# Kernel optimization log

Measured on AMD Instinct MI355X. Metric: run time of the kernel, lower is better.

## Reference

```python
import jax, jax.numpy as jnp
import numpy as np

N = 50000   # nodes
E = 600000  # edges (avg degree 12)
D = 128     # embedding_dim == hidden_features
L = 4       # depth


def setup_inputs() -> dict:
    key = jax.random.key(0)
    k0, k1, k2, k3 = jax.random.split(key, 4)
    scale = 1.0 / np.sqrt(D)
    node_embedding = jax.random.normal(k0, (N, D), jnp.float32)
    edge_index = jax.random.randint(k1, (2, E), 0, N, dtype=jnp.int32)
    Ws_rel = jax.random.normal(k2, (L, D, D), jnp.float32) * scale
    bs_rel = jnp.zeros((L, D), jnp.float32)
    Ws_root = jax.random.normal(k3, (L, D, D), jnp.float32) * scale
    return {
        'node_embedding': node_embedding,
        'edge_index': edge_index,
        'Ws_rel': Ws_rel,
        'bs_rel': bs_rel,
        'Ws_root': Ws_root,
    }


def reference(node_embedding, edge_index, Ws_rel, bs_rel, Ws_root):
    # PyG GraphConv (aggr='mean'), flow source_to_target:
    #   out_i = lin_rel(mean_{j in N(i)} x_j) + lin_root(x_i)
    # followed by ELU (dropout probs are 0 -> identity).
    n = node_embedding.shape[0]
    src, dst = edge_index[0], edge_index[1]
    ones = jnp.ones((edge_index.shape[1],), node_embedding.dtype)
    deg = jax.ops.segment_sum(ones, dst, num_segments=n)
    inv_deg = (1.0 / jnp.maximum(deg, 1.0))[:, None]  # [n, 1]
    X = node_embedding
    for l in range(Ws_rel.shape[0]):
        agg = jax.ops.segment_sum(X[src], dst, num_segments=n) * inv_deg  # [n, D]
        out = agg @ Ws_rel[l] + bs_rel[l] + X @ Ws_root[l]
        X = jax.nn.elu(out)
    return X
```

## Files before the change

kernel.cpp:

```cpp
#include <hip/hip_runtime.h>

#define D 128
#define LDR 264
#define TR 32
#define SLOTS 64
#define EPB 2048

typedef short bf16x8 __attribute__((ext_vector_type(8)));
typedef float f32x4 __attribute__((ext_vector_type(4)));

__device__ __forceinline__ unsigned short f2bf(float f) {
  unsigned int u = __float_as_uint(f);
  unsigned int r = (u + 0x7fff + ((u >> 16) & 1)) >> 16;
  return (unsigned short)r;
}
__device__ __forceinline__ unsigned int pack2bf(float lo, float hi) {
  return (unsigned int)f2bf(lo) | ((unsigned int)f2bf(hi) << 16);
}

__global__ __launch_bounds__(256) void k_build(
    const int* __restrict__ src, const int* __restrict__ dst, int E, int N,
    int* __restrict__ cursor, unsigned short* __restrict__ csr64,
    const float* __restrict__ X0, unsigned short* __restrict__ Xb, int total4,
    const float* __restrict__ Wrel, const float* __restrict__ Wroot,
    unsigned short* __restrict__ Wp, int wtot,
    int fb, int cb) {
  int b = blockIdx.x;
  if (b < fb) {
    int p = b & 7;
    int chunk = b >> 3;
    int lo = (int)((long long)p * N / 8);
    int hi = (int)((long long)(p + 1) * N / 8);
    int base = chunk * EPB + threadIdx.x;
#pragma unroll
    for (int it = 0; it < EPB / 256; ++it, base += 256) {
      if (base < E) {
        int d = dst[base];
        if (d >= lo && d < hi) {
          int ps = atomicAdd(&cursor[d], 1);
          if (ps < SLOTS) csr64[d * SLOTS + ps] = (unsigned short)src[base];
        }
      }
    }
    return;
  }
  b -= fb;
  if (b < cb) {
    int i = b * 256 + threadIdx.x;
    if (i < total4) {
      float4 v = ((const float4*)X0)[i];
      ushort4 o;
      o.x = f2bf(v.x); o.y = f2bf(v.y); o.z = f2bf(v.z); o.w = f2bf(v.w);
      ((ushort4*)Xb)[i] = o;
    }
    return;
  }
  b -= cb;
  {
    int gid = b * 256 + threadIdx.x;
    if (gid >= wtot) return;
    int lane = gid & 63;
    int t = gid >> 6;
    int ctg = t & 7; t >>= 3;
    int ks = t & 7; t >>= 3;
    int l = t;
    const float* Wr = Wrel + (size_t)l * D * D;
    const float* Wo = Wroot + (size_t)l * D * D;
    int colc = ctg * 16 + (lane & 15);
    int krow0 = ks * 32 + (lane >> 4) * 8;
    unsigned short tmp[8];
#pragma unroll
    for (int j = 0; j < 8; ++j) {
      int kr = krow0 + j;
      float w = (kr < D) ? Wr[(size_t)kr * D + colc] : Wo[(size_t)(kr - D) * D + colc];
      tmp[j] = f2bf(w);
    }
    unsigned short* dstp = Wp + ((size_t)gid) * 8;
#pragma unroll
    for (int j = 0; j < 8; ++j) dstp[j] = tmp[j];
  }
}


#define ACC8(v) \
    acc[0] += __uint_as_float((v).x << 16); acc[1] += __uint_as_float((v).x & 0xffff0000u); \
    acc[2] += __uint_as_float((v).y << 16); acc[3] += __uint_as_float((v).y & 0xffff0000u); \
    acc[4] += __uint_as_float((v).z << 16); acc[5] += __uint_as_float((v).z & 0xffff0000u); \
    acc[6] += __uint_as_float((v).w << 16); acc[7] += __uint_as_float((v).w & 0xffff0000u);

__global__ __launch_bounds__(256, 6) void k_layer_fused(
    const unsigned short* __restrict__ Xin,
    const int* __restrict__ cursor, const unsigned short* __restrict__ csr64,
    const unsigned short* __restrict__ Wp_l, const float* __restrict__ bias,
    unsigned short* __restrict__ Xnext, float* __restrict__ out_f32,
    int last, int N) {
  __shared__ __align__(16) unsigned short sRow[TR * LDR];
  int tid = threadIdx.x;
  int r0 = blockIdx.x * TR;
  int wave = tid >> 6, lane = tid & 63;
  int grp = lane >> 4;
  int l16 = lane & 15;

  int deg[2];
  uint2 bkt[2];
  uint4 vroot[2];
#pragma unroll
  for (int s = 0; s < 2; ++s) {
    int node = r0 + wave * 8 + s * 4 + grp;
    bool val = node < N;
    deg[s] = val ? cursor[node] : 0;
    bkt[s] = val ? *(const uint2*)(csr64 + (size_t)node * SLOTS + l16 * 4)
                 : make_uint2(0u, 0u);
    vroot[s] = val ? *(const uint4*)(Xin + (size_t)node * D + l16 * 8)
                   : make_uint4(0u, 0u, 0u, 0u);
  }

#pragma unroll
  for (int s = 0; s < 2; ++s) {
    int curnode = r0 + wave * 8 + s * 4 + grp;
    int safe = (curnode < N) ? curnode : 0;
    int r = wave * 8 + s * 4 + grp;
    *(uint4*)(&sRow[r * LDR + (16 + l16) * 8]) = vroot[s];

    float acc[8];
#pragma unroll
    for (int t = 0; t < 8; ++t) acc[t] = 0.f;

    int n = min(deg[s], SLOTS);
    int j = 0;
    for (; j < n; j += 8) {
      int rem = n - j;
      int a = grp * 16 + (j >> 2);
      unsigned ua_x = (unsigned)__shfl((int)bkt[s].x, a);
      unsigned ua_y = (unsigned)__shfl((int)bkt[s].y, a);
      if (rem > 4) {
        unsigned ub_x = (unsigned)__shfl((int)bkt[s].x, a + 1);
        unsigned ub_y = (unsigned)__shfl((int)bkt[s].y, a + 1);
        int e[8];
        e[0] = (int)(ua_x & 0xffffu); e[1] = (int)(ua_x >> 16);
        e[2] = (int)(ua_y & 0xffffu); e[3] = (int)(ua_y >> 16);
        e[4] = (int)(ub_x & 0xffffu); e[5] = (int)(ub_x >> 16);
        e[6] = (int)(ub_y & 0xffffu); e[7] = (int)(ub_y >> 16);
        uint4 vv[8];
#pragma unroll
        for (int t = 0; t < 8; ++t) {
          int idx = (j + t < n) ? e[t] : safe;
          vv[t] = *(const uint4*)(Xin + (size_t)idx * D + l16 * 8);
        }
#pragma unroll
        for (int t = 0; t < 8; ++t) {
          if (j + t < n) { ACC8(vv[t]) }
        }
      } else {
        int e[4];
        e[0] = (int)(ua_x & 0xffffu); e[1] = (int)(ua_x >> 16);
        e[2] = (int)(ua_y & 0xffffu); e[3] = (int)(ua_y >> 16);
        uint4 vv[4];
#pragma unroll
        for (int t = 0; t < 4; ++t) {
          int idx = (j + t < n) ? e[t] : safe;
          vv[t] = *(const uint4*)(Xin + (size_t)idx * D + l16 * 8);
        }
#pragma unroll
        for (int t = 0; t < 4; ++t) {
          if (j + t < n) { ACC8(vv[t]) }
        }
      }
    }

    float inv = 1.0f / fmaxf((float)deg[s], 1.0f);
    uint4 o;
    o.x = pack2bf(acc[0] * inv, acc[1] * inv);
    o.y = pack2bf(acc[2] * inv, acc[3] * inv);
    o.z = pack2bf(acc[4] * inv, acc[5] * inv);
    o.w = pack2bf(acc[6] * inv, acc[7] * inv);
    *(uint4*)(&sRow[r * LDR + l16 * 8]) = o;
  }
  __syncthreads();

  int m = l16, q = grp;
  int ct0 = wave * 2;

  f32x4 cacc[2][2];
#pragma unroll
  for (int g = 0; g < 2; ++g)
#pragma unroll
    for (int c = 0; c < 2; ++c) cacc[g][c] = (f32x4){0.f, 0.f, 0.f, 0.f};

  const unsigned short* arow = &sRow[m * LDR + q * 8];
#pragma unroll
  for (int ks = 0; ks < 8; ++ks) {
    bf16x8 b0 = *(const bf16x8*)(Wp_l + ((size_t)((ks * 8 + ct0 + 0) * 64 + lane)) * 8);
    bf16x8 b1 = *(const bf16x8*)(Wp_l + ((size_t)((ks * 8 + ct0 + 1) * 64 + lane)) * 8);
    bf16x8 a0 = *(const bf16x8*)(arow + ks * 32);
    bf16x8 a1 = *(const bf16x8*)(arow + 16 * LDR + ks * 32);
    cacc[0][0] = __builtin_amdgcn_mfma_f32_16x16x32_bf16(a0, b0, cacc[0][0], 0, 0, 0);
    cacc[0][1] = __builtin_amdgcn_mfma_f32_16x16x32_bf16(a0, b1, cacc[0][1], 0, 0, 0);
    cacc[1][0] = __builtin_amdgcn_mfma_f32_16x16x32_bf16(a1, b0, cacc[1][0], 0, 0, 0);
    cacc[1][1] = __builtin_amdgcn_mfma_f32_16x16x32_bf16(a1, b1, cacc[1][1], 0, 0, 0);
  }

#pragma unroll
  for (int g = 0; g < 2; ++g) {
#pragma unroll
    for (int c = 0; c < 2; ++c) {
      int col = (ct0 + c) * 16 + m;
      float bv = bias[col];
      int rbase = r0 + g * 16 + q * 4;
#pragma unroll
      for (int j = 0; j < 4; ++j) {
        int row = rbase + j;
        float v = cacc[g][c][j] + bv;
        float e = __expf(fminf(v, 0.f)) - 1.f;
        v = v > 0.f ? v : e;
        if (last) {
          if (row < N) out_f32[(size_t)row * D + col] = v;
        } else {
          unsigned int h = (unsigned int)f2bf(v);
          unsigned int nb = (unsigned int)__shfl_xor((int)h, 1);
          if (!(m & 1) && row < N)
            *(unsigned int*)(Xnext + (size_t)row * D + col) = h | (nb << 16);
        }
      }
    }
  }
}


extern "C" void kernel_launch(void* const* d_in, const int* in_sizes, int n_in,
                              void* d_out, int out_size, void* d_ws, size_t ws_size,
                              hipStream_t stream) {
  const float* X0    = (const float*)d_in[0];
  const int*   eidx  = (const int*)d_in[1];
  const float* Wrel  = (const float*)d_in[2];
  const float* brel  = (const float*)d_in[3];
  const float* Wroot = (const float*)d_in[4];
  float* out = (float*)d_out;

  const int N = in_sizes[0] / D;
  const int E = in_sizes[1] / 2;
  const int L = in_sizes[3] / D;
  const int* src = eidx;
  const int* dst = eidx + E;

  char* ws = (char*)d_ws;
  size_t off = 0;
  auto carve = [&](size_t bytes) -> void* {
    void* p = ws + off;
    off = (off + bytes + 255) & ~(size_t)255;
    return p;
  };
  unsigned short* Xb0  = (unsigned short*)carve((size_t)N * D * sizeof(unsigned short));
  unsigned short* Xb1  = (unsigned short*)carve((size_t)N * D * sizeof(unsigned short));
  unsigned short* Wp   = (unsigned short*)carve((size_t)L * 4096 * 8 * sizeof(unsigned short));
  int*            cursor = (int*)carve((size_t)N * sizeof(int));
  unsigned short* csr64  = (unsigned short*)carve((size_t)N * SLOTS * sizeof(unsigned short));
  (void)ws_size; (void)n_in; (void)out_size;

  hipMemsetAsync(cursor, 0, (size_t)N * sizeof(int), stream);

  const int chunks = (E + EPB - 1) / EPB;
  const int fb = chunks * 8;
  const int total4 = N * D / 4;
  const int cb = (total4 + 255) / 256;
  const int wtot = L * 4096;
  const int wb = (wtot + 255) / 256;
  k_build<<<fb + cb + wb, 256, 0, stream>>>(src, dst, E, N, cursor, csr64,
      X0, Xb0, total4, Wrel, Wroot, Wp, wtot, fb, cb);

  const int lb = (N + TR - 1) / TR;

  const unsigned short* Xcur = Xb0;
  for (int l = 0; l < L; ++l) {
    int last = (l == L - 1) ? 1 : 0;
    unsigned short* Xnext = (Xcur == Xb0) ? Xb1 : Xb0;
    k_layer_fused<<<lb, 256, 0, stream>>>(Xcur, cursor, csr64,
        Wp + (size_t)l * 4096 * 8, brel + (size_t)l * D, Xnext, out, last, N);
    Xcur = Xnext;
  }
}
```

Before: 236.9 us.

## Remap gather lanes: 8 nodes per wave, split neighbors and column chunks

Restructures the neighbor aggregation so that each wave handles 8 nodes at once. Each node gets 8 lanes: 4 column groups times 2 neighbor parities. The work loops over four 32-column chunks, processes neighbors in batches of 16 sized to the wave's maximum degree, and combines the parity halves with a shuffle-xor. Root rows are now staged into shared memory by a cooperative block-wide load. The intent is more outstanding gather loads per wave and less serialization on per-node degree, at the cost of re-reading the edge list per chunk, masked wasted lanes for low-degree nodes, and shuffle reductions.

New measurement: 267.8 us. 13.1% more time.

```diff
diff --git a/kernel.cpp b/kernel.cpp
--- a/kernel.cpp
+++ b/kernel.cpp
@@ -98,87 +98,73 @@
   int tid = threadIdx.x;
   int r0 = blockIdx.x * TR;
   int wave = tid >> 6, lane = tid & 63;
-  int grp = lane >> 4;
-  int l16 = lane & 15;
-
-  int deg[2];
-  uint2 bkt[2];
-  uint4 vroot[2];
-#pragma unroll
-  for (int s = 0; s < 2; ++s) {
-    int node = r0 + wave * 8 + s * 4 + grp;
-    bool val = node < N;
-    deg[s] = val ? cursor[node] : 0;
-    bkt[s] = val ? *(const uint2*)(csr64 + (size_t)node * SLOTS + l16 * 4)
-                 : make_uint2(0u, 0u);
-    vroot[s] = val ? *(const uint4*)(Xin + (size_t)node * D + l16 * 8)
+
+  for (int i = tid; i < TR * 16; i += 256) {
+    int r = i >> 4, c = i & 15;
+    int row = r0 + r;
+    uint4 v = make_uint4(0u, 0u, 0u, 0u);
+    if (row < N) v = *(const uint4*)(Xin + (size_t)row * D + c * 8);
+    *(uint4*)(&sRow[r * LDR + (16 + c) * 8]) = v;
+  }
+
+  int n  = lane >> 3;
+  int p  = (lane >> 2) & 1;
+  int l4 = lane & 3;
+  int node = r0 + wave * 8 + n;
+  bool nval = node < N;
+  int mydeg = nval ? cursor[node] : 0;
+  uint4 bkt = nval ? *(const uint4*)(csr64 + (size_t)node * SLOTS + (lane & 7) * 8)
                    : make_uint4(0u, 0u, 0u, 0u);
-  }
-
-#pragma unroll
-  for (int s = 0; s < 2; ++s) {
-    int curnode = r0 + wave * 8 + s * 4 + grp;
-    int safe = (curnode < N) ? curnode : 0;
-    int r = wave * 8 + s * 4 + grp;
-    *(uint4*)(&sRow[r * LDR + (16 + l16) * 8]) = vroot[s];
-
+  int ndeg = min(mydeg, SLOTS);
+  int md = ndeg;
+  md = max(md, __shfl_xor(md, 8));
+  md = max(md, __shfl_xor(md, 16));
+  md = max(md, __shfl_xor(md, 32));
+  int nbat = (md + 15) >> 4;
+  int sh = p * 16;
+
+#define LOADR(vv, RR, CMP, KOFF) { \
+    int j = jb + 2 * (RR) + p; \
+    unsigned bw = (unsigned)__shfl((int)(CMP), (n << 3) + b2 + (KOFF)); \
+    int e = (int)((bw >> sh) & 0xffffu); \
+    vv = make_uint4(0u, 0u, 0u, 0u); \
+    if (j < ndeg) vv = *(const uint4*)(Xcp + (size_t)e * D); }
+
+  for (int cp = 0; cp < 4; ++cp) {
+    const unsigned short* Xcp = Xin + cp * 32 + l4 * 8;
     float acc[8];
 #pragma unroll
     for (int t = 0; t < 8; ++t) acc[t] = 0.f;
 
-    int n = min(deg[s], SLOTS);
-    int j = 0;
-    for (; j < n; j += 8) {
-      int rem = n - j;
-      int a = grp * 16 + (j >> 2);
-      unsigned ua_x = (unsigned)__shfl((int)bkt[s].x, a);
-      unsigned ua_y = (unsigned)__shfl((int)bkt[s].y, a);
-      if (rem > 4) {
-        unsigned ub_x = (unsigned)__shfl((int)bkt[s].x, a + 1);
-        unsigned ub_y = (unsigned)__shfl((int)bkt[s].y, a + 1);
-        int e[8];
-        e[0] = (int)(ua_x & 0xffffu); e[1] = (int)(ua_x >> 16);
-        e[2] = (int)(ua_y & 0xffffu); e[3] = (int)(ua_y >> 16);
-        e[4] = (int)(ub_x & 0xffffu); e[5] = (int)(ub_x >> 16);
-        e[6] = (int)(ub_y & 0xffffu); e[7] = (int)(ub_y >> 16);
-        uint4 vv[8];
-#pragma unroll
-        for (int t = 0; t < 8; ++t) {
-          int idx = (j + t < n) ? e[t] : safe;
-          vv[t] = *(const uint4*)(Xin + (size_t)idx * D + l16 * 8);
-        }
-#pragma unroll
-        for (int t = 0; t < 8; ++t) {
-          if (j + t < n) { ACC8(vv[t]) }
-        }
-      } else {
-        int e[4];
-        e[0] = (int)(ua_x & 0xffffu); e[1] = (int)(ua_x >> 16);
-        e[2] = (int)(ua_y & 0xffffu); e[3] = (int)(ua_y >> 16);
-        uint4 vv[4];
-#pragma unroll
-        for (int t = 0; t < 4; ++t) {
-          int idx = (j + t < n) ? e[t] : safe;
-          vv[t] = *(const uint4*)(Xin + (size_t)idx * D + l16 * 8);
-        }
-#pragma unroll
-        for (int t = 0; t < 4; ++t) {
-          if (j + t < n) { ACC8(vv[t]) }
-        }
-      }
-    }
-
-    float inv = 1.0f / fmaxf((float)deg[s], 1.0f);
-    uint4 o;
-    o.x = pack2bf(acc[0] * inv, acc[1] * inv);
-    o.y = pack2bf(acc[2] * inv, acc[3] * inv);
-    o.z = pack2bf(acc[4] * inv, acc[5] * inv);
-    o.w = pack2bf(acc[6] * inv, acc[7] * inv);
-    *(uint4*)(&sRow[r * LDR + l16 * 8]) = o;
-  }
+    for (int b = 0; b < nbat; ++b) {
+      int jb = b * 16;
+      int b2 = b * 2;
+      uint4 v0, v1, v2, v3;
+      LOADR(v0, 0, bkt.x, 0) LOADR(v1, 1, bkt.y, 0)
+      LOADR(v2, 2, bkt.z, 0) LOADR(v3, 3, bkt.w, 0)
+      ACC8(v0) ACC8(v1) ACC8(v2) ACC8(v3)
+      LOADR(v0, 4, bkt.x, 1) LOADR(v1, 5, bkt.y, 1)
+      LOADR(v2, 6, bkt.z, 1) LOADR(v3, 7, bkt.w, 1)
+      ACC8(v0) ACC8(v1) ACC8(v2) ACC8(v3)
+    }
+
+#pragma unroll
+    for (int t = 0; t < 8; ++t) acc[t] += __shfl_xor(acc[t], 4);
+
+    if (p == 0) {
+      float inv = 1.0f / fmaxf((float)mydeg, 1.0f);
+      uint4 o;
+      o.x = pack2bf(acc[0] * inv, acc[1] * inv);
+      o.y = pack2bf(acc[2] * inv, acc[3] * inv);
+      o.z = pack2bf(acc[4] * inv, acc[5] * inv);
+      o.w = pack2bf(acc[6] * inv, acc[7] * inv);
+      *(uint4*)(&sRow[(wave * 8 + n) * LDR + (cp * 4 + l4) * 8]) = o;
+    }
+  }
+#undef LOADR
   __syncthreads();
 
-  int m = l16, q = grp;
+  int m = lane & 15, q = lane >> 4;
   int ct0 = wave * 2;
 
   f32x4 cacc[2][2];
```
